# Optimization experiments

Hardware: AMD Instinct MI355X
Metric: run time of the kernel (lower is better)

Reference implementation:

```python
import jax, jax.numpy as jnp
import numpy as np

N_NODES = 100000
N_EDGES = 1000000
D = 64  # gat_input_size == gat_hidden_size
NEG_SLOPE = 0.2  # PyG GATConv default leaky_relu slope


def setup_inputs() -> dict:
    key = jax.random.key(0)
    k1, k2, k3, k4, k5, k6 = jax.random.split(key, 6)
    g = jax.random.normal(k1, (N_NODES, D), dtype=jnp.float32)
    edge_index = jax.random.randint(k2, (2, N_EDGES), 0, N_NODES, dtype=jnp.int32)
    scale = 1.0 / np.sqrt(D)
    W = jax.random.normal(k3, (D, D), dtype=jnp.float32) * scale
    att_src = jax.random.normal(k4, (D,), dtype=jnp.float32) * scale
    att_dst = jax.random.normal(k5, (D,), dtype=jnp.float32) * scale
    bias = jnp.zeros((D,), dtype=jnp.float32)
    return {"g": g, "edge_index": edge_index, "W": W,
            "att_src": att_src, "att_dst": att_dst, "bias": bias}


def _gat_layer(x, src, dst, W, att_src, att_dst, bias):
    N = x.shape[0]
    h = x @ W                               # [N, D] projected features
    a_src = h @ att_src                     # [N] per-node source logits
    a_dst = h @ att_dst                     # [N] per-node target logits
    e = jax.nn.leaky_relu(a_src[src] + a_dst[dst], NEG_SLOPE)  # [E]
    # numerically stable segment softmax over edges grouped by target node
    m = jax.ops.segment_max(e, dst, num_segments=N)            # [N]
    m = jnp.where(jnp.isfinite(m), m, 0.0)                     # isolated nodes
    ex = jnp.exp(e - m[dst])                                   # [E]
    denom = jax.ops.segment_sum(ex, dst, num_segments=N)       # [N]
    alpha = ex / (denom[dst] + 1e-16)                          # [E]
    out = jax.ops.segment_sum(alpha[:, None] * h[src], dst, num_segments=N)
    return out + bias


def reference(g, edge_index, W, att_src, att_dst, bias):
    src, dst = edge_index[0], edge_index[1]
    for _ in range(4):  # same shared GAT applied 4 times
        g = _gat_layer(g, src, dst, W, att_src, att_dst, bias)
    return g
```

## Files before the change

kernel.cpp:

```cpp
#include <hip/hip_runtime.h>
#include <hip/hip_bf16.h>

typedef unsigned int u32;
typedef unsigned short u16;
typedef unsigned long long u64;
typedef __attribute__((ext_vector_type(8))) short short8;
typedef __attribute__((ext_vector_type(4))) float f32x4;

#define LRELU_SLOPE 0.2f
#define BPB 32
#define MAXPER 13000

__device__ inline float bfbits(u32 hi) { union { u32 i; float f; } v; v.i = hi; return v.f; }
__device__ inline float bflo(u32 w) { return bfbits(w << 16); }
__device__ inline float bfhi(u32 w) { return bfbits(w & 0xFFFF0000u); }
__device__ inline float bf2f(u16 s) { return bfbits(((u32)s) << 16); }
__device__ inline u16 f2bf(float f) {
  union { float f; u32 i; } v; v.f = f;
  u32 r = v.i + 0x7FFFu + ((v.i >> 16) & 1u);
  return (u16)(r >> 16);
}

__global__ void dp_kernel(const u32* __restrict__ g, int nwords, int* __restrict__ mode,
                          const void* __restrict__ W, const void* __restrict__ as,
                          const void* __restrict__ ad, const void* __restrict__ bs,
                          float* __restrict__ pf, u16* __restrict__ wfrag) {
  __shared__ int cnt;
  if (threadIdx.x == 0) cnt = 0;
  __syncthreads();
  int c = 0;
  for (int i = threadIdx.x; i < nwords; i += 256) {
    u32 e = g[i] & 0x7F80u;
    if (e >= 0x3000u && e <= 0x4180u) c++;
  }
  atomicAdd(&cnt, c);
  __syncthreads();
  int md = (2 * cnt > nwords) ? 1 : 0;
  if (threadIdx.x == 0) *mode = md;

  for (int i = threadIdx.x; i < 4288; i += 256) {
    const void* p; int j;
    if (i < 4096)      { p = W;  j = i; }
    else if (i < 4160) { p = as; j = i - 4096; }
    else if (i < 4224) { p = ad; j = i - 4160; }
    else               { p = bs; j = i - 4224; }
    pf[i] = md ? bf2f(((const u16*)p)[j]) : ((const float*)p)[j];
  }
  __syncthreads();
  for (int i = threadIdx.x; i < 4096; i += 256) {
    int f = i >> 9, lane = (i >> 3) & 63, j = i & 7;
    int cc = f >> 1, t = f & 1;
    int k = 32 * t + 8 * (lane >> 4) + j;
    int n = 16 * cc + (lane & 15);
    wfrag[i] = f2bf(pf[k * 64 + n]);
  }
}

__global__ void conv_x_kernel(const void* __restrict__ g, u16* __restrict__ x, int n,
                              const int* __restrict__ mode) {
  if (*mode) return;
  int stride = gridDim.x * blockDim.x;
  for (int i = blockIdx.x * blockDim.x + threadIdx.x; i < n; i += stride)
    x[i] = f2bf(((const float*)g)[i]);
}

__global__ void __launch_bounds__(256) binA_kernel(
    const int* __restrict__ src, const int* __restrict__ dst, int* __restrict__ gcnt,
    uint2* __restrict__ binned, int E, int nper, int cap) {
  __shared__ int lcnt[8], lbase[8], lcur[8];
  const int K = 8;
  int tile0 = blockIdx.x * (256 * K);
  int t = threadIdx.x;
  if (t < 8) { lcnt[t] = 0; lcur[t] = 0; }
  __syncthreads();
  int dv[K], sv[K], bv[K];
#pragma unroll
  for (int j = 0; j < K; ++j) {
    int idx = tile0 + j * 256 + t;
    bool ok = idx < E;
    int d = ok ? __builtin_nontemporal_load(&dst[idx]) : 0;
    int s = ok ? __builtin_nontemporal_load(&src[idx]) : 0;
    int b = -1;
    if (ok) {
      b = (d >= 4 * nper) ? 4 : 0;
      if (d >= (b + 2) * nper) b += 2;
      if (d >= (b + 1) * nper) b += 1;
      atomicAdd(&lcnt[b], 1);
    }
    dv[j] = d; sv[j] = s; bv[j] = b;
  }
  __syncthreads();
  if (t < 8) lbase[t] = atomicAdd(&gcnt[t], lcnt[t]);
  __syncthreads();
#pragma unroll
  for (int j = 0; j < K; ++j) {
    int b = bv[j];
    if (b >= 0) {
      int slot = lbase[b] + atomicAdd(&lcur[b], 1);
      if (slot < cap) binned[(size_t)b * cap + slot] = make_uint2((u32)sv[j], (u32)dv[j]);
    }
  }
}

__global__ void __launch_bounds__(256) histA_kernel(
    const uint2* __restrict__ binned, const int* __restrict__ gcnt,
    u32* __restrict__ slices, int nper, int cap) {
  __shared__ u32 cnt_lds[MAXPER];
  int b = blockIdx.x & 7;
  int j = blockIdx.x >> 3;
  int cnt = gcnt[b]; if (cnt > cap) cnt = cap;
  int chunk = (cnt + BPB - 1) / BPB;
  int begin = j * chunk;
  int endc = begin + chunk; if (endc > cnt) endc = cnt;
  for (int k = threadIdx.x; k < nper; k += 256) cnt_lds[k] = 0;
  __syncthreads();
  const uint2* reg = binned + (size_t)b * cap;
  int kbase = b * nper;
  for (int i = begin + threadIdx.x; i < endc; i += 256)
    atomicAdd(&cnt_lds[(int)reg[i].y - kbase], 1u);
  __syncthreads();
  u32* out = slices + (size_t)(b * BPB + j) * nper;
  for (int k = threadIdx.x; k < nper; k += 256) out[k] = cnt_lds[k];
}

__global__ void scan1f_kernel(const u32* __restrict__ slices, int* __restrict__ row_off,
                              int* __restrict__ partials, int nper, int N) {
  __shared__ int smem[1024];
  int t = threadIdx.x;
  int idx = blockIdx.x * 1024 + t;
  int v = 0;
  if (idx < N) {
    int b = idx / nper;
    int kk = idx - b * nper;
    const u32* s = slices + (size_t)b * BPB * nper + kk;
    u32 tt = 0;
#pragma unroll 8
    for (int j = 0; j < BPB; ++j) tt += s[(size_t)j * nper];
    v = (int)tt;
  }
  smem[t] = v;
  __syncthreads();
  for (int off = 1; off < 1024; off <<= 1) {
    int u = (t >= off) ? smem[t - off] : 0;
    __syncthreads();
    smem[t] += u;
    __syncthreads();
  }
  if (idx < N) row_off[idx + 1] = smem[t];
  if (t == 1023) partials[blockIdx.x] = smem[t];
}

__global__ void scan2_kernel(int* __restrict__ partials, int P) {
  __shared__ int smem[1024];
  int t = threadIdx.x;
  int v = (t < P) ? partials[t] : 0;
  smem[t] = v;
  __syncthreads();
  for (int off = 1; off < 1024; off <<= 1) {
    int u = (t >= off) ? smem[t - off] : 0;
    __syncthreads();
    smem[t] += u;
    __syncthreads();
  }
  if (t < P) partials[t] = smem[t];
}

__global__ void scan3b_kernel(int* __restrict__ row_off, const int* __restrict__ partials,
                              u32* __restrict__ slices, int nper, int N) {
  int blk = blockIdx.x;
  int idx = blk * 1024 + threadIdx.x;
  if (idx == 0) row_off[0] = 0;
  if (idx < N) {
    int v = row_off[idx + 1] + ((blk > 0) ? partials[blk - 1] : 0);
    row_off[idx + 1] = v;
    int b = idx / nper;
    int kk = idx - b * nper;
    u32* s = slices + (size_t)b * BPB * nper + kk;
    u32 run = (u32)v;
#pragma unroll 8
    for (int j = BPB - 1; j >= 0; --j) {
      u32 tt = s[(size_t)j * nper];
      run -= tt;
      s[(size_t)j * nper] = run;
    }
  }
}

__global__ void __launch_bounds__(256) scatterB_kernel(
    const uint2* __restrict__ binned, const int* __restrict__ gcnt,
    const u32* __restrict__ slices, int* __restrict__ csr_src, int nper, int cap) {
  __shared__ u32 base_lds[MAXPER];
  int b = blockIdx.x & 7;
  int j = blockIdx.x >> 3;
  int cnt = gcnt[b]; if (cnt > cap) cnt = cap;
  int chunk = (cnt + BPB - 1) / BPB;
  int begin = j * chunk;
  int endc = begin + chunk; if (endc > cnt) endc = cnt;
  const u32* s = slices + (size_t)(b * BPB + j) * nper;
  for (int k = threadIdx.x; k < nper; k += 256) base_lds[k] = s[k];
  __syncthreads();
  const uint2* reg = binned + (size_t)b * cap;
  int kbase = b * nper;
  for (int i = begin + threadIdx.x; i < endc; i += 256) {
    uint2 r = reg[i];
    u32 p = atomicAdd(&base_lds[(int)r.y - kbase], 1u);
    csr_src[p] = (int)r.x;
  }
}

__global__ void hist_local_kernel(const uint2* __restrict__ binned, const int* __restrict__ gcnt,
                                  int* __restrict__ deg, int cap) {
  int b = blockIdx.x & 7;
  int vb = blockIdx.x >> 3, nvb = gridDim.x >> 3;
  int cnt = gcnt[b]; if (cnt > cap) cnt = cap;
  const uint2* reg = binned + (size_t)b * cap;
  for (int i = vb * blockDim.x + threadIdx.x; i < cnt; i += nvb * blockDim.x)
    atomicAdd(&deg[reg[i].y], 1);
}

__global__ void scatter_local_kernel(const uint2* __restrict__ binned, const int* __restrict__ gcnt,
                                     int* __restrict__ cursor, int* __restrict__ csr_src, int cap) {
  int b = blockIdx.x & 7;
  int vb = blockIdx.x >> 3, nvb = gridDim.x >> 3;
  int cnt = gcnt[b]; if (cnt > cap) cnt = cap;
  const uint2* reg = binned + (size_t)b * cap;
  for (int i = vb * blockDim.x + threadIdx.x; i < cnt; i += nvb * blockDim.x) {
    uint2 r = reg[i];
    int p = atomicAdd(&cursor[r.y], 1);
    csr_src[p] = (int)r.x;
  }
}

__global__ void scan1_kernel(const int* __restrict__ deg, int* __restrict__ row_off,
                             int* __restrict__ partials, int N) {
  __shared__ int smem[1024];
  int t = threadIdx.x;
  int idx = blockIdx.x * 1024 + t;
  int v = (idx < N) ? deg[idx] : 0;
  smem[t] = v;
  __syncthreads();
  for (int off = 1; off < 1024; off <<= 1) {
    int u = (t >= off) ? smem[t - off] : 0;
    __syncthreads();
    smem[t] += u;
    __syncthreads();
  }
  if (idx < N) row_off[idx + 1] = smem[t];
  if (t == 1023) partials[blockIdx.x] = smem[t];
}

__global__ void scan3_kernel(int* __restrict__ row_off, const int* __restrict__ partials,
                             int* __restrict__ cursor, int N) {
  int b = blockIdx.x;
  int idx = b * 1024 + threadIdx.x;
  if (idx < N) {
    int v = row_off[idx + 1] + ((b > 0) ? partials[b - 1] : 0);
    row_off[idx + 1] = v;
    if (idx + 1 < N) cursor[idx + 1] = v;
  }
  if (idx == 0) { row_off[0] = 0; cursor[0] = 0; }
}

__global__ void __launch_bounds__(256) proj_mfma_kernel(
    const u16* __restrict__ x, const void* __restrict__ graw, const int* __restrict__ mode,
    int first, const u16* __restrict__ wfrag, const float* __restrict__ pf,
    u16* __restrict__ h, float* __restrict__ a_src, float* __restrict__ a_dst, int N) {
  int lane = threadIdx.x & 63;
  int quad = lane >> 4, m = lane & 15;
  int wtile = (int)((blockIdx.x * (size_t)blockDim.x + threadIdx.x) >> 6);
  int ntiles = (N + 15) >> 4;
  int nwaves = (int)((gridDim.x * (size_t)blockDim.x) >> 6);

  const u16* xin = (first && *mode) ? (const u16*)graw : x;

  short8 bfrag[8];
#pragma unroll
  for (int f = 0; f < 8; ++f)
    bfrag[f] = *(const short8*)(wfrag + f * 512 + lane * 8);
  float asv[4], adv[4];
#pragma unroll
  for (int c = 0; c < 4; ++c) {
    asv[c] = pf[4096 + 16 * c + m];
    adv[c] = pf[4160 + 16 * c + m];
  }

  for (int tile = wtile; tile < ntiles; tile += nwaves) {
    int row0 = tile << 4;
    int rl = row0 + m; if (rl > N - 1) rl = N - 1;
    const u16* xr = xin + (size_t)rl * 64 + 8 * quad;
    short8 a0 = *(const short8*)(xr);
    short8 a1 = *(const short8*)(xr + 32);

    f32x4 acc[4];
#pragma unroll
    for (int c = 0; c < 4; ++c) {
      f32x4 z = {0.f, 0.f, 0.f, 0.f};
      z = __builtin_amdgcn_mfma_f32_16x16x32_bf16(a0, bfrag[2 * c + 0], z, 0, 0, 0);
      z = __builtin_amdgcn_mfma_f32_16x16x32_bf16(a1, bfrag[2 * c + 1], z, 0, 0, 0);
      acc[c] = z;
    }

#pragma unroll
    for (int r = 0; r < 4; ++r) {
      int row = row0 + 4 * quad + r;
      float v0 = acc[0][r], v1 = acc[1][r], v2 = acc[2][r], v3 = acc[3][r];
      if (row < N) {
        u16* hr = h + (size_t)row * 64 + m;
        hr[0]  = f2bf(v0);
        hr[16] = f2bf(v1);
        hr[32] = f2bf(v2);
        hr[48] = f2bf(v3);
      }
      float s1 = v0 * asv[0] + v1 * asv[1] + v2 * asv[2] + v3 * asv[3];
      float s2 = v0 * adv[0] + v1 * adv[1] + v2 * adv[2] + v3 * adv[3];
#pragma unroll
      for (int msk = 1; msk <= 8; msk <<= 1) {
        s1 += __shfl_xor(s1, msk, 64);
        s2 += __shfl_xor(s2, msk, 64);
      }
      if (m == 0 && row < N) { a_src[row] = s1; a_dst[row] = s2; }
    }
  }
}

__global__ void __launch_bounds__(256) gather_kernel(
    const u16* __restrict__ h, const float* __restrict__ a_src,
    const float* __restrict__ a_dst, const int* __restrict__ row_off,
    const int* __restrict__ csr_src, const float* __restrict__ pf,
    u16* __restrict__ xout, void* __restrict__ dout, int N, int last,
    const int* __restrict__ mode) {
  int lane = threadIdx.x & 63;
  int grp = lane >> 4;
  int eg  = (lane >> 3) & 1;
  int fg  = lane & 7;
  int wid = (int)((blockIdx.x * blockDim.x + threadIdx.x) >> 6);
  int i0 = wid * 4;
  if (i0 >= N) return;
  int i = i0 + grp;
  bool valid = i < N;

  int beg = 0, end = 0;
  float adv = 0.f;
  if (valid) {
    beg = row_off[i];
    end = row_off[i + 1];
    adv = a_dst[i];
  }

  float acc[8] = {0.f, 0.f, 0.f, 0.f, 0.f, 0.f, 0.f, 0.f};
  float den = 0.f;

  if (beg < end) {
    int lastE = end - 1;
    for (int b0 = beg; b0 < end; b0 += 8) {
      int eA = b0 + eg;
      int eB = b0 + 2 + eg;
      int eC = b0 + 4 + eg;
      int eD = b0 + 6 + eg;
      float vA = (eA < end) ? 1.f : 0.f;
      float vB = (eB < end) ? 1.f : 0.f;
      float vC = (eC < end) ? 1.f : 0.f;
      float vD = (eD < end) ? 1.f : 0.f;
      int sA = csr_src[(eA < end) ? eA : lastE];
      int sB = csr_src[(eB < end) ? eB : lastE];
      int sC = csr_src[(eC < end) ? eC : lastE];
      int sD = csr_src[(eD < end) ? eD : lastE];
      float aA = a_src[sA];
      float aB = a_src[sB];
      float aC = a_src[sC];
      float aD = a_src[sD];
      uint4 hA = ((const uint4*)(h + (size_t)sA * 64))[fg];
      uint4 hB = ((const uint4*)(h + (size_t)sB * 64))[fg];
      uint4 hC = ((const uint4*)(h + (size_t)sC * 64))[fg];
      uint4 hD = ((const uint4*)(h + (size_t)sD * 64))[fg];

      float tA = aA + adv; tA = (tA > 0.f) ? tA : LRELU_SLOPE * tA;
      float tB = aB + adv; tB = (tB > 0.f) ? tB : LRELU_SLOPE * tB;
      float tC = aC + adv; tC = (tC > 0.f) ? tC : LRELU_SLOPE * tC;
      float tD = aD + adv; tD = (tD > 0.f) ? tD : LRELU_SLOPE * tD;
      float wA = __expf(fminf(tA, 60.f)) * vA;
      float wB = __expf(fminf(tB, 60.f)) * vB;
      float wC = __expf(fminf(tC, 60.f)) * vC;
      float wD = __expf(fminf(tD, 60.f)) * vD;
      den += (wA + wB) + (wC + wD);
      acc[0] += wA * bflo(hA.x) + wB * bflo(hB.x) + wC * bflo(hC.x) + wD * bflo(hD.x);
      acc[1] += wA * bfhi(hA.x) + wB * bfhi(hB.x) + wC * bfhi(hC.x) + wD * bfhi(hD.x);
      acc[2] += wA * bflo(hA.y) + wB * bflo(hB.y) + wC * bflo(hC.y) + wD * bflo(hD.y);
      acc[3] += wA * bfhi(hA.y) + wB * bfhi(hB.y) + wC * bfhi(hC.y) + wD * bfhi(hD.y);
      acc[4] += wA * bflo(hA.z) + wB * bflo(hB.z) + wC * bflo(hC.z) + wD * bflo(hD.z);
      acc[5] += wA * bfhi(hA.z) + wB * bfhi(hB.z) + wC * bfhi(hC.z) + wD * bfhi(hD.z);
      acc[6] += wA * bflo(hA.w) + wB * bflo(hB.w) + wC * bflo(hC.w) + wD * bflo(hD.w);
      acc[7] += wA * bfhi(hA.w) + wB * bfhi(hB.w) + wC * bfhi(hC.w) + wD * bfhi(hD.w);
    }
  }

  den += __shfl_xor(den, 8, 64);
#pragma unroll
  for (int j = 0; j < 8; ++j) acc[j] += __shfl_xor(acc[j], 8, 64);
  float inv = (den > 0.f) ? 1.f / den : 0.f;

  if (!valid || eg) return;

  if (*mode || !last) {
    u32 o[4];
#pragma unroll
    for (int j = 0; j < 4; ++j) {
      float f0 = acc[2 * j]     * inv + pf[4224 + 8 * fg + 2 * j];
      float f1 = acc[2 * j + 1] * inv + pf[4224 + 8 * fg + 2 * j + 1];
      o[j] = (u32)f2bf(f0) | ((u32)f2bf(f1) << 16);
    }
    u16* base = last ? (u16*)dout : xout;
    *(uint4*)(base + (size_t)i * 64 + fg * 8) = make_uint4(o[0], o[1], o[2], o[3]);
  } else {
    float o[8];
#pragma unroll
    for (int j = 0; j < 8; ++j)
      o[j] = acc[j] * inv + pf[4224 + 8 * fg + j];
    float* dp = (float*)dout + (size_t)i * 64 + fg * 8;
    *(float4*)(dp)     = make_float4(o[0], o[1], o[2], o[3]);
    *(float4*)(dp + 4) = make_float4(o[4], o[5], o[6], o[7]);
  }
}

extern "C" void kernel_launch(void* const* d_in, const int* in_sizes, int n_in,
                              void* d_out, int out_size, void* d_ws, size_t ws_size,
                              hipStream_t stream) {
  const void* g     = d_in[0];
  const int*  edge  = (const int*)d_in[1];
  const void* Wp    = d_in[2];
  const void* attsp = d_in[3];
  const void* attdp = d_in[4];
  const void* biasp = d_in[5];

  const int D = 64;
  const int N = in_sizes[0] / D;
  const int E = in_sizes[1] / 2;
  const int* src = edge;
  const int* dst = edge + E;

  int nper = (N + 7) / 8;
  bool fast_csr = (nper <= MAXPER);

  char* ws = (char*)d_ws;
  size_t off = 0;
  auto alloc = [&](size_t bytes) -> char* {
    char* p = ws + off;
    off += (bytes + 255) & ~size_t(255);
    return p;
  };
  size_t h_bytes = (size_t)N * D * sizeof(u16);
  size_t slice_bytes = (size_t)8 * BPB * nper * sizeof(u32);
  u16*   x        = (u16*)alloc((size_t)N * D * sizeof(u16));
  u16*   h        = (u16*)alloc(h_bytes > slice_bytes ? h_bytes : slice_bytes);
  u32*   slices   = (u32*)h;
  float* pf       = (float*)alloc(4288 * sizeof(float));
  u16*   wfrag    = (u16*)alloc(4096 * sizeof(u16));
  float* a_src    = (float*)alloc((size_t)N * sizeof(float));
  float* a_dst    = (float*)alloc((size_t)N * sizeof(float));
  int*   deg      = (int*)alloc((size_t)N * sizeof(int));
  int*   row_off  = (int*)alloc((size_t)(N + 1) * sizeof(int));
  int*   cursor   = (int*)alloc((size_t)N * sizeof(int));
  int*   csr_src  = (int*)alloc((size_t)E * sizeof(int));
  int*   partials = (int*)alloc(1024 * sizeof(int));
  int*   mode     = (int*)alloc(256);
  int*   gcnt     = (int*)alloc(256);
  int    cap      = E / 8 + 16384;
  uint2* binned   = (uint2*)alloc((size_t)8 * cap * sizeof(uint2));

  dp_kernel<<<1, 256, 0, stream>>>((const u32*)g, 4096, mode, Wp, attsp, attdp, biasp,
                                   pf, wfrag);

  int n64 = N * D;
  int cblocks = (n64 + 255) / 256; if (cblocks > 2048) cblocks = 2048;
  conv_x_kernel<<<cblocks, 256, 0, stream>>>(g, x, n64, mode);

  hipMemsetAsync(gcnt, 0, 8 * sizeof(int), stream);
  if (!fast_csr) hipMemsetAsync(deg, 0, (size_t)N * sizeof(int), stream);
  int abl = (E + 2047) / 2048;
  binA_kernel<<<abl, 256, 0, stream>>>(src, dst, gcnt, binned, E, nper, cap);

  int nblk = (N + 1023) / 1024;
  if (fast_csr) {
    histA_kernel<<<8 * BPB, 256, 0, stream>>>(binned, gcnt, slices, nper, cap);
    scan1f_kernel<<<nblk, 1024, 0, stream>>>(slices, row_off, partials, nper, N);
    scan2_kernel<<<1, 1024, 0, stream>>>(partials, nblk);
    scan3b_kernel<<<nblk, 1024, 0, stream>>>(row_off, partials, slices, nper, N);
    scatterB_kernel<<<8 * BPB, 256, 0, stream>>>(binned, gcnt, slices, csr_src, nper, cap);
  } else {
    hist_local_kernel<<<1024, 256, 0, stream>>>(binned, gcnt, deg, cap);
    scan1_kernel<<<nblk, 1024, 0, stream>>>(deg, row_off, partials, N);
    scan2_kernel<<<1, 1024, 0, stream>>>(partials, nblk);
    scan3_kernel<<<nblk, 1024, 0, stream>>>(row_off, partials, cursor, N);
    scatter_local_kernel<<<1024, 256, 0, stream>>>(binned, gcnt, cursor, csr_src, cap);
  }

  int ntiles = (N + 15) / 16;
  int tblocks = (ntiles + 3) / 4;
  for (int layer = 0; layer < 4; ++layer) {
    proj_mfma_kernel<<<tblocks, 256, 0, stream>>>(x, g, mode, layer == 0 ? 1 : 0,
                                                  wfrag, pf, h, a_src, a_dst, N);
    int last = (layer == 3) ? 1 : 0;
    gather_kernel<<<(N + 15) / 16, 256, 0, stream>>>(h, a_src, a_dst, row_off, csr_src, pf,
                                                     x, d_out, N, last, mode);
  }
}
```

Baseline: 311.8 us.

## Pad CSR rows to multiples of eight with dummy node; fold conversion and scans

Each CSR row is padded to a multiple of 8 edges using a dummy source node N, which has zero features and a -1e30 logit. The gather loop can then drop its per-edge bounds checks and validity masks, and its accumulation is rewritten with packed float2 FMAs. The fp32-to-bf16 input conversion kernel and the gcnt memset are folded into the layer-0 projection and dp kernels, and scan2 is merged into scan3. In exchange the gather does extra memory traffic and exp work on padding edges, and csr_src grows.

```diff
diff --git a/kernel.cpp b/kernel.cpp
--- a/kernel.cpp
+++ b/kernel.cpp
@@ -6,6 +6,7 @@
 typedef unsigned long long u64;
 typedef __attribute__((ext_vector_type(8))) short short8;
 typedef __attribute__((ext_vector_type(4))) float f32x4;
+typedef __attribute__((ext_vector_type(2))) float f32x2;
 
 #define LRELU_SLOPE 0.2f
 #define BPB 32
@@ -20,13 +21,16 @@
   u32 r = v.i + 0x7FFFu + ((v.i >> 16) & 1u);
   return (u16)(r >> 16);
 }
+__device__ inline f32x2 up2(u32 w) { return (f32x2){bflo(w), bfhi(w)}; }
 
 __global__ void dp_kernel(const u32* __restrict__ g, int nwords, int* __restrict__ mode,
                           const void* __restrict__ W, const void* __restrict__ as,
                           const void* __restrict__ ad, const void* __restrict__ bs,
-                          float* __restrict__ pf, u16* __restrict__ wfrag) {
+                          float* __restrict__ pf, u16* __restrict__ wfrag,
+                          int* __restrict__ gcnt) {
   __shared__ int cnt;
   if (threadIdx.x == 0) cnt = 0;
+  if (threadIdx.x < 8) gcnt[threadIdx.x] = 0;
   __syncthreads();
   int c = 0;
   for (int i = threadIdx.x; i < nwords; i += 256) {
@@ -54,14 +58,6 @@
     int n = 16 * cc + (lane & 15);
     wfrag[i] = f2bf(pf[k * 64 + n]);
   }
-}
-
-__global__ void conv_x_kernel(const void* __restrict__ g, u16* __restrict__ x, int n,
-                              const int* __restrict__ mode) {
-  if (*mode) return;
-  int stride = gridDim.x * blockDim.x;
-  for (int i = blockIdx.x * blockDim.x + threadIdx.x; i < n; i += stride)
-    x[i] = f2bf(((const float*)g)[i]);
 }
 
 __global__ void __launch_bounds__(256) binA_kernel(
@@ -136,7 +132,7 @@
     u32 tt = 0;
 #pragma unroll 8
     for (int j = 0; j < BPB; ++j) tt += s[(size_t)j * nper];
-    v = (int)tt;
+    v = (int)((tt + 7u) & ~7u);
   }
   smem[t] = v;
   __syncthreads();
@@ -150,11 +146,13 @@
   if (t == 1023) partials[blockIdx.x] = smem[t];
 }
 
-__global__ void scan2_kernel(int* __restrict__ partials, int P) {
+__global__ void scan3c_kernel(int* __restrict__ row_off, const int* __restrict__ partials,
+                              int P, u32* __restrict__ slices, int* __restrict__ csr_src,
+                              int nper, int N, int dummy) {
   __shared__ int smem[1024];
   int t = threadIdx.x;
-  int v = (t < P) ? partials[t] : 0;
-  smem[t] = v;
+  int pv = (t < P) ? partials[t] : 0;
+  smem[t] = pv;
   __syncthreads();
   for (int off = 1; off < 1024; off <<= 1) {
     int u = (t >= off) ? smem[t - off] : 0;
@@ -162,27 +160,25 @@
     smem[t] += u;
     __syncthreads();
   }
-  if (t < P) partials[t] = smem[t];
-}
-
-__global__ void scan3b_kernel(int* __restrict__ row_off, const int* __restrict__ partials,
-                              u32* __restrict__ slices, int nper, int N) {
   int blk = blockIdx.x;
-  int idx = blk * 1024 + threadIdx.x;
+  int prefix = (blk > 0) ? smem[blk - 1] : 0;
+  int idx = blk * 1024 + t;
   if (idx == 0) row_off[0] = 0;
   if (idx < N) {
-    int v = row_off[idx + 1] + ((blk > 0) ? partials[blk - 1] : 0);
-    row_off[idx + 1] = v;
+    int vend = row_off[idx + 1] + prefix;
+    row_off[idx + 1] = vend;
     int b = idx / nper;
     int kk = idx - b * nper;
     u32* s = slices + (size_t)b * BPB * nper + kk;
-    u32 run = (u32)v;
-#pragma unroll 8
-    for (int j = BPB - 1; j >= 0; --j) {
-      u32 tt = s[(size_t)j * nper];
-      run -= tt;
-      s[(size_t)j * nper] = run;
-    }
+    u32 tv[BPB];
+    u32 deg = 0;
+#pragma unroll
+    for (int j = 0; j < BPB; ++j) { tv[j] = s[(size_t)j * nper]; deg += tv[j]; }
+    u32 pdeg = (deg + 7u) & ~7u;
+    u32 run = (u32)vend - pdeg;
+#pragma unroll
+    for (int j = 0; j < BPB; ++j) { s[(size_t)j * nper] = run; run += tv[j]; }
+    for (u32 p = run; p < (u32)vend; ++p) csr_src[p] = dummy;
   }
 }
 
@@ -236,7 +232,7 @@
   __shared__ int smem[1024];
   int t = threadIdx.x;
   int idx = blockIdx.x * 1024 + t;
-  int v = (idx < N) ? deg[idx] : 0;
+  int v = (idx < N) ? (int)(((u32)deg[idx] + 7u) & ~7u) : 0;
   smem[t] = v;
   __syncthreads();
   for (int off = 1; off < 1024; off <<= 1) {
@@ -247,6 +243,21 @@
   }
   if (idx < N) row_off[idx + 1] = smem[t];
   if (t == 1023) partials[blockIdx.x] = smem[t];
+}
+
+__global__ void scan2_kernel(int* __restrict__ partials, int P) {
+  __shared__ int smem[1024];
+  int t = threadIdx.x;
+  int v = (t < P) ? partials[t] : 0;
+  smem[t] = v;
+  __syncthreads();
+  for (int off = 1; off < 1024; off <<= 1) {
+    int u = (t >= off) ? smem[t - off] : 0;
+    __syncthreads();
+    smem[t] += u;
+    __syncthreads();
+  }
+  if (t < P) partials[t] = smem[t];
 }
 
 __global__ void scan3_kernel(int* __restrict__ row_off, const int* __restrict__ partials,
@@ -261,17 +272,31 @@
   if (idx == 0) { row_off[0] = 0; cursor[0] = 0; }
 }
 
+__global__ void padC_kernel(const int* __restrict__ row_off, const int* __restrict__ cursor,
+                            int* __restrict__ csr_src, int N, int dummy) {
+  int i = blockIdx.x * blockDim.x + threadIdx.x;
+  if (i >= N) return;
+  int e = row_off[i + 1];
+  for (int p = cursor[i]; p < e; ++p) csr_src[p] = dummy;
+}
+
 __global__ void __launch_bounds__(256) proj_mfma_kernel(
     const u16* __restrict__ x, const void* __restrict__ graw, const int* __restrict__ mode,
     int first, const u16* __restrict__ wfrag, const float* __restrict__ pf,
     u16* __restrict__ h, float* __restrict__ a_src, float* __restrict__ a_dst, int N) {
+  if (blockIdx.x == 0) {
+    if (threadIdx.x < 32) ((u32*)(h + (size_t)N * 64))[threadIdx.x] = 0u;
+    else if (threadIdx.x == 32) a_src[N] = -1e30f;
+  }
   int lane = threadIdx.x & 63;
   int quad = lane >> 4, m = lane & 15;
   int wtile = (int)((blockIdx.x * (size_t)blockDim.x + threadIdx.x) >> 6);
   int ntiles = (N + 15) >> 4;
   int nwaves = (int)((gridDim.x * (size_t)blockDim.x) >> 6);
 
-  const u16* xin = (first && *mode) ? (const u16*)graw : x;
+  int md = *mode;
+  bool f32in = (first && md == 0);
+  const u16* xin = (first && md) ? (const u16*)graw : x;
 
   short8 bfrag[8];
 #pragma unroll
@@ -287,9 +312,26 @@
   for (int tile = wtile; tile < ntiles; tile += nwaves) {
     int row0 = tile << 4;
     int rl = row0 + m; if (rl > N - 1) rl = N - 1;
-    const u16* xr = xin + (size_t)rl * 64 + 8 * quad;
-    short8 a0 = *(const short8*)(xr);
-    short8 a1 = *(const short8*)(xr + 32);
+    short8 a0, a1;
+    if (f32in) {
+      const float* xr = (const float*)graw + (size_t)rl * 64 + 8 * quad;
+      float4 f0 = *(const float4*)(xr);
+      float4 f1 = *(const float4*)(xr + 4);
+      float4 f2 = *(const float4*)(xr + 32);
+      float4 f3 = *(const float4*)(xr + 36);
+      a0[0] = (short)f2bf(f0.x); a0[1] = (short)f2bf(f0.y);
+      a0[2] = (short)f2bf(f0.z); a0[3] = (short)f2bf(f0.w);
+      a0[4] = (short)f2bf(f1.x); a0[5] = (short)f2bf(f1.y);
+      a0[6] = (short)f2bf(f1.z); a0[7] = (short)f2bf(f1.w);
+      a1[0] = (short)f2bf(f2.x); a1[1] = (short)f2bf(f2.y);
+      a1[2] = (short)f2bf(f2.z); a1[3] = (short)f2bf(f2.w);
+      a1[4] = (short)f2bf(f3.x); a1[5] = (short)f2bf(f3.y);
+      a1[6] = (short)f2bf(f3.z); a1[7] = (short)f2bf(f3.w);
+    } else {
+      const u16* xr = xin + (size_t)rl * 64 + 8 * quad;
+      a0 = *(const short8*)(xr);
+      a1 = *(const short8*)(xr + 32);
+    }
 
     f32x4 acc[4];
 #pragma unroll
@@ -347,66 +389,63 @@
     adv = a_dst[i];
   }
 
-  float acc[8] = {0.f, 0.f, 0.f, 0.f, 0.f, 0.f, 0.f, 0.f};
+  f32x2 acc0 = {0.f, 0.f}, acc1 = {0.f, 0.f}, acc2 = {0.f, 0.f}, acc3 = {0.f, 0.f};
   float den = 0.f;
 
-  if (beg < end) {
-    int lastE = end - 1;
-    for (int b0 = beg; b0 < end; b0 += 8) {
-      int eA = b0 + eg;
-      int eB = b0 + 2 + eg;
-      int eC = b0 + 4 + eg;
-      int eD = b0 + 6 + eg;
-      float vA = (eA < end) ? 1.f : 0.f;
-      float vB = (eB < end) ? 1.f : 0.f;
-      float vC = (eC < end) ? 1.f : 0.f;
-      float vD = (eD < end) ? 1.f : 0.f;
-      int sA = csr_src[(eA < end) ? eA : lastE];
-      int sB = csr_src[(eB < end) ? eB : lastE];
-      int sC = csr_src[(eC < end) ? eC : lastE];
-      int sD = csr_src[(eD < end) ? eD : lastE];
-      float aA = a_src[sA];
-      float aB = a_src[sB];
-      float aC = a_src[sC];
-      float aD = a_src[sD];
-      uint4 hA = ((const uint4*)(h + (size_t)sA * 64))[fg];
-      uint4 hB = ((const uint4*)(h + (size_t)sB * 64))[fg];
-      uint4 hC = ((const uint4*)(h + (size_t)sC * 64))[fg];
-      uint4 hD = ((const uint4*)(h + (size_t)sD * 64))[fg];
-
-      float tA = aA + adv; tA = (tA > 0.f) ? tA : LRELU_SLOPE * tA;
-      float tB = aB + adv; tB = (tB > 0.f) ? tB : LRELU_SLOPE * tB;
-      float tC = aC + adv; tC = (tC > 0.f) ? tC : LRELU_SLOPE * tC;
-      float tD = aD + adv; tD = (tD > 0.f) ? tD : LRELU_SLOPE * tD;
-      float wA = __expf(fminf(tA, 60.f)) * vA;
-      float wB = __expf(fminf(tB, 60.f)) * vB;
-      float wC = __expf(fminf(tC, 60.f)) * vC;
-      float wD = __expf(fminf(tD, 60.f)) * vD;
-      den += (wA + wB) + (wC + wD);
-      acc[0] += wA * bflo(hA.x) + wB * bflo(hB.x) + wC * bflo(hC.x) + wD * bflo(hD.x);
-      acc[1] += wA * bfhi(hA.x) + wB * bfhi(hB.x) + wC * bfhi(hC.x) + wD * bfhi(hD.x);
-      acc[2] += wA * bflo(hA.y) + wB * bflo(hB.y) + wC * bflo(hC.y) + wD * bflo(hD.y);
-      acc[3] += wA * bfhi(hA.y) + wB * bfhi(hB.y) + wC * bfhi(hC.y) + wD * bfhi(hD.y);
-      acc[4] += wA * bflo(hA.z) + wB * bflo(hB.z) + wC * bflo(hC.z) + wD * bflo(hD.z);
-      acc[5] += wA * bfhi(hA.z) + wB * bfhi(hB.z) + wC * bfhi(hC.z) + wD * bfhi(hD.z);
-      acc[6] += wA * bflo(hA.w) + wB * bflo(hB.w) + wC * bflo(hC.w) + wD * bflo(hD.w);
-      acc[7] += wA * bfhi(hA.w) + wB * bfhi(hB.w) + wC * bfhi(hC.w) + wD * bfhi(hD.w);
-    }
+  for (int b0 = beg; b0 < end; b0 += 8) {
+    int eA = b0 + eg;
+    int sA = csr_src[eA];
+    int sB = csr_src[eA + 2];
+    int sC = csr_src[eA + 4];
+    int sD = csr_src[eA + 6];
+    float aA = a_src[sA];
+    float aB = a_src[sB];
+    float aC = a_src[sC];
+    float aD = a_src[sD];
+    uint4 hA = ((const uint4*)(h + (size_t)sA * 64))[fg];
+    uint4 hB = ((const uint4*)(h + (size_t)sB * 64))[fg];
+    uint4 hC = ((const uint4*)(h + (size_t)sC * 64))[fg];
+    uint4 hD = ((const uint4*)(h + (size_t)sD * 64))[fg];
+
+    float tA = aA + adv; tA = (tA > 0.f) ? tA : LRELU_SLOPE * tA;
+    float tB = aB + adv; tB = (tB > 0.f) ? tB : LRELU_SLOPE * tB;
+    float tC = aC + adv; tC = (tC > 0.f) ? tC : LRELU_SLOPE * tC;
+    float tD = aD + adv; tD = (tD > 0.f) ? tD : LRELU_SLOPE * tD;
+    float wA = __expf(fminf(tA, 60.f));
+    float wB = __expf(fminf(tB, 60.f));
+    float wC = __expf(fminf(tC, 60.f));
+    float wD = __expf(fminf(tD, 60.f));
+    den += (wA + wB) + (wC + wD);
+    f32x2 wA2 = {wA, wA}, wB2 = {wB, wB}, wC2 = {wC, wC}, wD2 = {wD, wD};
+    acc0 += wA2 * up2(hA.x); acc0 += wB2 * up2(hB.x);
+    acc0 += wC2 * up2(hC.x); acc0 += wD2 * up2(hD.x);
+    acc1 += wA2 * up2(hA.y); acc1 += wB2 * up2(hB.y);
+    acc1 += wC2 * up2(hC.y); acc1 += wD2 * up2(hD.y);
+    acc2 += wA2 * up2(hA.z); acc2 += wB2 * up2(hB.z);
+    acc2 += wC2 * up2(hC.z); acc2 += wD2 * up2(hD.z);
+    acc3 += wA2 * up2(hA.w); acc3 += wB2 * up2(hB.w);
+    acc3 += wC2 * up2(hC.w); acc3 += wD2 * up2(hD.w);
   }
 
   den += __shfl_xor(den, 8, 64);
 #pragma unroll
-  for (int j = 0; j < 8; ++j) acc[j] += __shfl_xor(acc[j], 8, 64);
+  for (int c = 0; c < 2; ++c) {
+    acc0[c] += __shfl_xor(acc0[c], 8, 64);
+    acc1[c] += __shfl_xor(acc1[c], 8, 64);
+    acc2[c] += __shfl_xor(acc2[c], 8, 64);
+    acc3[c] += __shfl_xor(acc3[c], 8, 64);
+  }
   float inv = (den > 0.f) ? 1.f / den : 0.f;
 
   if (!valid || eg) return;
 
+  float oa[8] = {acc0[0], acc0[1], acc1[0], acc1[1], acc2[0], acc2[1], acc3[0], acc3[1]};
   if (*mode || !last) {
     u32 o[4];
 #pragma unroll
     for (int j = 0; j < 4; ++j) {
-      float f0 = acc[2 * j]     * inv + pf[4224 + 8 * fg + 2 * j];
-      float f1 = acc[2 * j + 1] * inv + pf[4224 + 8 * fg + 2 * j + 1];
+      float f0 = oa[2 * j]     * inv + pf[4224 + 8 * fg + 2 * j];
+      float f1 = oa[2 * j + 1] * inv + pf[4224 + 8 * fg + 2 * j + 1];
       o[j] = (u32)f2bf(f0) | ((u32)f2bf(f1) << 16);
     }
     u16* base = last ? (u16*)dout : xout;
@@ -415,7 +454,7 @@
     float o[8];
 #pragma unroll
     for (int j = 0; j < 8; ++j)
-      o[j] = acc[j] * inv + pf[4224 + 8 * fg + j];
+      o[j] = oa[j] * inv + pf[4224 + 8 * fg + j];
     float* dp = (float*)dout + (size_t)i * 64 + fg * 8;
     *(float4*)(dp)     = make_float4(o[0], o[1], o[2], o[3]);
     *(float4*)(dp + 4) = make_float4(o[4], o[5], o[6], o[7]);
@@ -448,19 +487,19 @@
     off += (bytes + 255) & ~size_t(255);
     return p;
   };
-  size_t h_bytes = (size_t)N * D * sizeof(u16);
+  size_t h_bytes = (size_t)(N + 1) * D * sizeof(u16);
   size_t slice_bytes = (size_t)8 * BPB * nper * sizeof(u32);
   u16*   x        = (u16*)alloc((size_t)N * D * sizeof(u16));
   u16*   h        = (u16*)alloc(h_bytes > slice_bytes ? h_bytes : slice_bytes);
   u32*   slices   = (u32*)h;
   float* pf       = (float*)alloc(4288 * sizeof(float));
   u16*   wfrag    = (u16*)alloc(4096 * sizeof(u16));
-  float* a_src    = (float*)alloc((size_t)N * sizeof(float));
+  float* a_src    = (float*)alloc((size_t)(N + 1) * sizeof(float));
   float* a_dst    = (float*)alloc((size_t)N * sizeof(float));
   int*   deg      = (int*)alloc((size_t)N * sizeof(int));
   int*   row_off  = (int*)alloc((size_t)(N + 1) * sizeof(int));
   int*   cursor   = (int*)alloc((size_t)N * sizeof(int));
-  int*   csr_src  = (int*)alloc((size_t)E * sizeof(int));
+  int*   csr_src  = (int*)alloc(((size_t)E + 8 * (size_t)N) * sizeof(int));
   int*   partials = (int*)alloc(1024 * sizeof(int));
   int*   mode     = (int*)alloc(256);
   int*   gcnt     = (int*)alloc(256);
@@ -468,13 +507,8 @@
   uint2* binned   = (uint2*)alloc((size_t)8 * cap * sizeof(uint2));
 
   dp_kernel<<<1, 256, 0, stream>>>((const u32*)g, 4096, mode, Wp, attsp, attdp, biasp,
-                                   pf, wfrag);
-
-  int n64 = N * D;
-  int cblocks = (n64 + 255) / 256; if (cblocks > 2048) cblocks = 2048;
-  conv_x_kernel<<<cblocks, 256, 0, stream>>>(g, x, n64, mode);
-
-  hipMemsetAsync(gcnt, 0, 8 * sizeof(int), stream);
+                                   pf, wfrag, gcnt);
+
   if (!fast_csr) hipMemsetAsync(deg, 0, (size_t)N * sizeof(int), stream);
   int abl = (E + 2047) / 2048;
   binA_kernel<<<abl, 256, 0, stream>>>(src, dst, gcnt, binned, E, nper, cap);
@@ -483,8 +517,8 @@
   if (fast_csr) {
     histA_kernel<<<8 * BPB, 256, 0, stream>>>(binned, gcnt, slices, nper, cap);
     scan1f_kernel<<<nblk, 1024, 0, stream>>>(slices, row_off, partials, nper, N);
-    scan2_kernel<<<1, 1024, 0, stream>>>(partials, nblk);
-    scan3b_kernel<<<nblk, 1024, 0, stream>>>(row_off, partials, slices, nper, N);
+    scan3c_kernel<<<nblk, 1024, 0, stream>>>(row_off, partials, nblk, slices, csr_src,
+                                             nper, N, N);
     scatterB_kernel<<<8 * BPB, 256, 0, stream>>>(binned, gcnt, slices, csr_src, nper, cap);
   } else {
     hist_local_kernel<<<1024, 256, 0, stream>>>(binned, gcnt, deg, cap);
@@ -492,6 +526,7 @@
     scan2_kernel<<<1, 1024, 0, stream>>>(partials, nblk);
     scan3_kernel<<<nblk, 1024, 0, stream>>>(row_off, partials, cursor, N);
     scatter_local_kernel<<<1024, 256, 0, stream>>>(binned, gcnt, cursor, csr_src, cap);
+    padC_kernel<<<(N + 255) / 256, 256, 0, stream>>>(row_off, cursor, csr_src, N, N);
   }
 
   int ntiles = (N + 15) / 16;
```

After: 280.2 us. -10.1%, faster.
